# Kernel optimization log

Measured on AMD Instinct MI355X. Metric: run time of the kernel, lower is better.

The kernel has to match this reference:

```python
import jax, jax.numpy as jnp
import numpy as np

B, C, H, W = 32, 3, 256, 256
P = 32        # patch_size
NP = 4        # num_patches
STRENGTH = 0.1  # adversarial_strength default


def _conv2d(x, w, b):
    # NCHW conv, 3x3, stride 1, padding 1 ('SAME')
    y = jax.lax.conv_general_dilated(
        x, w, window_strides=(1, 1), padding='SAME',
        dimension_numbers=('NCHW', 'OIHW', 'NCHW'))
    return y + b[None, :, None, None]


def setup_inputs() -> dict:
    key = jax.random.key(0)
    ks = jax.random.split(key, 12)
    s = 0.05
    return {
        'x':   jax.random.normal(ks[0], (B, C, H, W), jnp.float32),
        # selected bit-width patch generator (bits_8): conv C->32->16->C
        'w1':  jax.random.normal(ks[1], (32, C, 3, 3), jnp.float32) * s,
        'b1':  jnp.zeros((32,), jnp.float32),
        'w2':  jax.random.normal(ks[2], (16, 32, 3, 3), jnp.float32) * s,
        'b2':  jnp.zeros((16,), jnp.float32),
        'w3':  jax.random.normal(ks[3], (C, 16, 3, 3), jnp.float32) * s,
        'b3':  jnp.zeros((C,), jnp.float32),
        # position predictor: Linear(C*64 -> 128) then Linear(128 -> NP*2)
        'pw1': jax.random.normal(ks[4], (128, C * 64), jnp.float32) * s,
        'pb1': jnp.zeros((128,), jnp.float32),
        'pw2': jax.random.normal(ks[5], (NP * 2, 128), jnp.float32) * s,
        'pb2': jnp.zeros((NP * 2,), jnp.float32),
        'bit_width': 8,
    }


def reference(x, w1, b1, w2, b2, w3, b3, pw1, pb1, pw2, pb2, bit_width):
    # patch generator for the selected bit width (bit_width selects a ModuleDict
    # entry in torch; all entries have identical structure, one set of weights here)
    h1 = jax.nn.relu(_conv2d(x, w1, b1))          # [B,32,H,W]
    h2 = jax.nn.relu(_conv2d(h1, w2, b2))         # [B,16,H,W]
    patches = jnp.tanh(_conv2d(h2, w3, b3)) * STRENGTH  # [B,C,H,W]

    # position predictor: AdaptiveAvgPool2d((8,8)) -> flatten -> MLP -> sigmoid
    pooled = x.reshape(B, C, 8, H // 8, 8, W // 8).mean(axis=(3, 5))  # [B,C,8,8]
    feat = pooled.reshape(B, -1)                                       # [B,C*64]
    hmid = jax.nn.relu(feat @ pw1.T + pb1)
    pos = jax.nn.sigmoid(hmid @ pw2.T + pb2).reshape(B, NP, 2)

    # int() truncation of sigmoid-scaled positions (nonnegative -> floor)
    y0 = jnp.floor(pos[..., 0] * (H - P)).astype(jnp.int32)  # [B,NP]
    x0 = jnp.floor(pos[..., 1] * (W - P)).astype(jnp.int32)  # [B,NP]

    ar = jnp.arange(P, dtype=jnp.int32)
    rows = y0[:, :, None, None] + ar[None, None, :, None]    # [B,NP,P,P]
    cols = x0[:, :, None, None] + ar[None, None, None, :]    # [B,NP,P,P]
    bidx = jnp.arange(B, dtype=jnp.int32)[:, None, None, None]  # [B,1,1,1]

    # gather patch values at the same windows, then scatter-add into x.
    # advanced idx (bidx, rows, cols) around the channel slice -> [B,NP,P,P,C];
    # duplicate (overlapping) windows accumulate, matching sequential += in torch.
    vals = patches[bidx, :, rows, cols]
    patched_x = x.at[bidx, :, rows, cols].add(vals)
    return patched_x
```

## Files before the change

### kernel.cpp

```cpp
#include <hip/hip_runtime.h>
#include <math.h>

#define BATCH 32
#define CH 3
#define HH 256
#define WW 256
#define PP 32
#define NPATCH 4

typedef __attribute__((ext_vector_type(8))) short short8;
typedef __attribute__((ext_vector_type(4))) float f32x4;

__device__ __forceinline__ unsigned short f2bf(float f) {
  union { float f; unsigned u; } cv;
  cv.f = f;
  unsigned u = cv.u;
  u += 0x7FFFu + ((u >> 16) & 1u);
  return (unsigned short)(u >> 16);
}

__global__ __launch_bounds__(256) void prep_kernel(
    const float* __restrict__ x, float* __restrict__ out,
    float* __restrict__ feat, const float* __restrict__ w1,
    const float* __restrict__ w2, const float* __restrict__ w3,
    const float* __restrict__ pw1, unsigned short* __restrict__ w1f,
    unsigned short* __restrict__ w2f, unsigned short* __restrict__ w3f,
    float* __restrict__ pw1t) {
  const int blk = blockIdx.x;
  const int t = threadIdx.x;

  if (blk >= 792) {
    const int seg = blk - 792;
#pragma unroll
    for (int q = 0; q < 4; ++q) {
      int idx = seg * 1024 + q * 256 + t;
      if (idx < 1024) {
        int nt = idx >> 9, lane_ = (idx >> 3) & 63, j = idx & 7;
        int lrow_ = lane_ & 15, lgrp_ = lane_ >> 4;
        int k = lgrp_ * 8 + j;
        w1f[idx] = f2bf(k < 27 ? w1[(nt * 16 + lrow_) * 27 + k] : 0.f);
      } else if (idx < 5632) {
        int id2 = idx - 1024;
        int tap = id2 >> 9, lane_ = (id2 >> 3) & 63, j = id2 & 7;
        int lrow_ = lane_ & 15, lgrp_ = lane_ >> 4;
        w2f[id2] = f2bf(w2[lrow_ * 288 + (lgrp_ * 8 + j) * 9 + tap]);
      } else if (idx < 8192) {
        int id3 = idx - 5632;
        int kk = id3 >> 9, lane_ = (id3 >> 3) & 63, j = id3 & 7;
        int lrow_ = lane_ & 15, lgrp_ = lane_ >> 4;
        int tap = 2 * kk + (lgrp_ >> 1);
        int c2 = (lgrp_ & 1) * 8 + j;
        float v = (lrow_ < 3 && tap < 9) ? w3[lrow_ * 144 + c2 * 9 + tap] : 0.f;
        w3f[id3] = f2bf(v);
      }
    }
    return;
  }

  if (blk >= 768) {
    const int tile = blk - 768;
    const int ko = (tile % 6) * 32;
    const int to = (tile / 6) * 32;
    __shared__ float tl[32][33];
    int ty = t >> 5, tx = t & 31;
#pragma unroll
    for (int r = 0; r < 4; ++r) {
      int row = r * 8 + ty;
      tl[row][tx] = pw1[(to + row) * 192 + ko + tx];
    }
    __syncthreads();
#pragma unroll
    for (int r = 0; r < 4; ++r) {
      int row = r * 8 + ty;
      pw1t[(ko + row) * 128 + to + tx] = tl[tx][row];
    }
    return;
  }

  const int b = blk / 24;
  const int rem = blk - b * 24;
  const int c = rem >> 3;
  const int i = rem & 7;
  const int wv = t >> 6;
  const int lane = t & 63;
  const int j = lane >> 3;

  __shared__ float part[32];

  const size_t base4 = ((size_t)((b * 3 + c) * 256 + i * 32)) * 64;
  float s = 0.f;
#pragma unroll
  for (int k = 0; k < 8; ++k) {
    int r = k * 4 + wv;
    size_t F = base4 + (size_t)r * 64 + lane;
    float4 v = ((const float4*)x)[F];
    ((float4*)out)[F] = v;
    s += v.x + v.y + v.z + v.w;
  }
  s += __shfl_xor(s, 1, 64);
  s += __shfl_xor(s, 2, 64);
  s += __shfl_xor(s, 4, 64);
  if ((lane & 7) == 0) part[wv * 8 + j] = s;
  __syncthreads();
  if (t < 8) {
    float tot = part[t] + part[8 + t] + part[16 + t] + part[24 + t];
    feat[b * 192 + c * 64 + i * 8 + t] = tot * (1.f / 1024.f);
  }
}

__global__ __launch_bounds__(256) void mlp_kernel(
    const float* __restrict__ feat, const float* __restrict__ pw1t,
    const float* __restrict__ pb1, const float* __restrict__ pw2,
    const float* __restrict__ pb2, int* __restrict__ posw) {
  const int b = blockIdx.x;
  const int t = threadIdx.x;
  __shared__ float fs[192];
  __shared__ float part[2][128];
  __shared__ float hs[128];

  if (t < 192) fs[t] = feat[b * 192 + t];
  __syncthreads();

  {
    const int u = t & 127, h = t >> 7;
    float a0 = 0.f, a1 = 0.f;
    const float* wp = pw1t + (h * 96) * 128 + u;
    const float* fp = fs + h * 96;
#pragma unroll 12
    for (int k = 0; k < 96; k += 2) {
      a0 = fmaf(fp[k], wp[k * 128], a0);
      a1 = fmaf(fp[k + 1], wp[(k + 1) * 128], a1);
    }
    part[h][u] = a0 + a1;
  }
  __syncthreads();
  if (t < 128) hs[t] = fmaxf(part[0][t] + part[1][t] + pb1[t], 0.f);
  __syncthreads();

  const int wv = t >> 6, hl = (t >> 5) & 1, l = t & 31;
  const int jj = wv * 2 + hl;
  float a = 0.f;
#pragma unroll
  for (int q = 0; q < 4; ++q)
    a = fmaf(hs[q * 32 + l], pw2[jj * 128 + q * 32 + l], a);
#pragma unroll
  for (int m = 1; m <= 16; m <<= 1) a += __shfl_xor(a, m, 32);
  if (l == 0) {
    float a2 = a + pb2[jj];
    float sgm = 1.f / (1.f + expf(-a2));
    posw[b * 8 + jj] = (int)floorf(sgm * (float)(HH - PP));
  }
}

__global__ __launch_bounds__(512, 4) void patch_kernel(
    const float* __restrict__ x, float* __restrict__ out,
    const float* __restrict__ b1, const float* __restrict__ b2,
    const float* __restrict__ b3, const int* __restrict__ posw,
    const unsigned short* __restrict__ w1f, const unsigned short* __restrict__ w2f,
    const unsigned short* __restrict__ w3f) {
  const int blk = blockIdx.x;
  const int s = blk & 3;
  const int p = (blk >> 2) & 3;
  const int b = blk >> 4;
  const int rb = s * 8;
  const int t = threadIdx.x;
  const int wv = t >> 6;
  const int lane = t & 63;
  const int lrow = lane & 15;
  const int lgrp = lane >> 4;

  __shared__ __align__(16) float xs[3][532];
  __shared__ __align__(16) unsigned short buf[432 * 40];
  __shared__ __align__(16) unsigned short h2ls[352 * 16];

  const int y0 = posw[b * 8 + p * 2 + 0];
  const int x0 = posw[b * 8 + p * 2 + 1];

#pragma unroll
  for (int k = 0; k < 4; ++k) {
    int idx = t + 512 * k;
    if (idx < 1596) {
      int c = idx / 532;
      int r = idx - c * 532;
      int ky = r / 38, kx = r - (r / 38) * 38;
      int gy = y0 + rb - 3 + ky, gx = x0 - 3 + kx;
      float v = 0.f;
      if ((unsigned)gy < 256u && (unsigned)gx < 256u)
        v = x[((size_t)(b * 3 + c) * 256 + gy) * 256 + gx];
      xs[c][r] = v;
    }
  }

  short8 b1f[2], b2f[9], b3f[5];
#pragma unroll
  for (int nt = 0; nt < 2; ++nt)
    b1f[nt] = *(const short8*)&w1f[(nt * 64 + lane) * 8];
#pragma unroll
  for (int tap = 0; tap < 9; ++tap)
    b2f[tap] = *(const short8*)&w2f[(tap * 64 + lane) * 8];
#pragma unroll
  for (int kk = 0; kk < 5; ++kk)
    b3f[kk] = *(const short8*)&w3f[(kk * 64 + lane) * 8];
  float b1v0 = b1[lrow], b1v1 = b1[16 + lrow];
  float bias2 = b2[lrow];
  float bias3 = (lrow < 3) ? b3[lrow] : 0.f;

  __syncthreads();

  if (t < 432) {
    int pos = t;
    int jy = pos / 36, jx = pos - (pos / 36) * 36;
    unsigned short cv[32];
#pragma unroll
    for (int c = 0; c < 3; ++c)
#pragma unroll
      for (int dy = 0; dy < 3; ++dy)
#pragma unroll
        for (int dx = 0; dx < 3; ++dx)
          cv[c * 9 + dy * 3 + dx] = f2bf(xs[c][(jy + dy) * 38 + (jx + dx)]);
#pragma unroll
    for (int k = 27; k < 32; ++k) cv[k] = 0;
#pragma unroll
    for (int qq = 0; qq < 4; ++qq) {
      short8 v8;
#pragma unroll
      for (int j = 0; j < 8; ++j) v8[j] = (short)cv[qq * 8 + j];
      *(short8*)&buf[pos * 40 + qq * 8] = v8;
    }
  }
  __syncthreads();

  f32x4 acc1[4][2];
#pragma unroll
  for (int i = 0; i < 4; ++i) {
    int mt = wv + 8 * i;
    if (mt < 27) {
      short8 a = *(const short8*)&buf[(mt * 16 + lrow) * 40 + lgrp * 8];
      f32x4 z = f32x4{0.f, 0.f, 0.f, 0.f};
#pragma unroll
      for (int nt = 0; nt < 2; ++nt)
        acc1[i][nt] = __builtin_amdgcn_mfma_f32_16x16x32_bf16(a, b1f[nt], z, 0, 0, 0);
    }
  }
  __syncthreads();

#pragma unroll
  for (int i = 0; i < 4; ++i) {
    int mt = wv + 8 * i;
    if (mt < 27) {
#pragma unroll
      for (int r = 0; r < 4; ++r) {
        int pos = mt * 16 + lgrp * 4 + r;
        int jy = pos / 36, jx = pos - (pos / 36) * 36;
        bool inim = ((unsigned)(y0 + rb - 2 + jy) < 256u) &&
                    ((unsigned)(x0 - 2 + jx) < 256u);
#pragma unroll
        for (int nt = 0; nt < 2; ++nt) {
          float v = fmaxf(acc1[i][nt][r] + (nt ? b1v1 : b1v0), 0.f);
          buf[pos * 40 + nt * 16 + lrow] = inim ? f2bf(v) : (unsigned short)0;
        }
      }
    }
  }
  __syncthreads();

  f32x4 acc[3];
#pragma unroll
  for (int i = 0; i < 3; ++i) {
    int mt = wv + 8 * i;
    if (mt < 22) {
      int pos = mt * 16 + lrow;
      int posc = pos < 340 ? pos : 339;
      int iy = posc / 34, ix = posc - (posc / 34) * 34;
      const unsigned short* abase = &buf[(iy * 36 + ix) * 40 + lgrp * 8];
      f32x4 c = f32x4{0.f, 0.f, 0.f, 0.f};
#pragma unroll
      for (int dy = 0; dy < 3; ++dy)
#pragma unroll
        for (int dx = 0; dx < 3; ++dx) {
          short8 a = *(const short8*)(abase + (dy * 36 + dx) * 40);
          c = __builtin_amdgcn_mfma_f32_16x16x32_bf16(a, b2f[dy * 3 + dx], c, 0, 0, 0);
        }
      acc[i] = c;
    } else {
      acc[i] = f32x4{0.f, 0.f, 0.f, 0.f};
    }
  }
#pragma unroll
  for (int i = 0; i < 3; ++i) {
    int mt = wv + 8 * i;
    if (mt < 22) {
#pragma unroll
      for (int r = 0; r < 4; ++r) {
        int pos = mt * 16 + lgrp * 4 + r;
        if (pos < 340) {
          int iy = pos / 34, ix = pos - (pos / 34) * 34;
          bool inim = ((unsigned)(y0 + rb - 1 + iy) < 256u) &&
                      ((unsigned)(x0 - 1 + ix) < 256u);
          float v = fmaxf(acc[i][r] + bias2, 0.f);
          h2ls[pos * 16 + lrow] = inim ? f2bf(v) : (unsigned short)0;
        }
      }
    }
  }
  __syncthreads();

  f32x4 acc3[2];
#pragma unroll
  for (int i = 0; i < 2; ++i) {
    int mt = wv * 2 + i;
    int pix = mt * 16 + lrow;
    int oy = pix >> 5, ox = pix & 31;
    f32x4 c = f32x4{0.f, 0.f, 0.f, 0.f};
#pragma unroll
    for (int kk = 0; kk < 5; ++kk) {
      int tap = 2 * kk + (lgrp >> 1);
      short8 a = short8{0, 0, 0, 0, 0, 0, 0, 0};
      if (tap < 9) {
        int dy = (tap * 11) >> 5;
        int dx = tap - dy * 3;
        a = *(const short8*)&h2ls[((oy + dy) * 34 + (ox + dx)) * 16 + (lgrp & 1) * 8];
      }
      c = __builtin_amdgcn_mfma_f32_16x16x32_bf16(a, b3f[kk], c, 0, 0, 0);
    }
    acc3[i] = c;
  }
  if (lrow < 3) {
#pragma unroll
    for (int i = 0; i < 2; ++i) {
      int mt = wv * 2 + i;
#pragma unroll
      for (int r = 0; r < 4; ++r) {
        int pix = mt * 16 + lgrp * 4 + r;
        int oy = pix >> 5, ox = pix & 31;
        float v = acc3[i][r] + bias3;
        float e = __expf(2.f * v);
        float val = (1.f - 2.f / (e + 1.f)) * 0.1f;
        atomicAdd(&out[((size_t)(b * 3 + lrow) * 256 + (y0 + rb + oy)) * 256 +
                       (x0 + ox)],
                  val);
      }
    }
  }
}

extern "C" void kernel_launch(void* const* d_in, const int* in_sizes, int n_in,
                              void* d_out, int out_size, void* d_ws, size_t ws_size,
                              hipStream_t stream) {
  const float* x   = (const float*)d_in[0];
  const float* w1  = (const float*)d_in[1];
  const float* b1  = (const float*)d_in[2];
  const float* w2  = (const float*)d_in[3];
  const float* b2  = (const float*)d_in[4];
  const float* w3  = (const float*)d_in[5];
  const float* b3  = (const float*)d_in[6];
  const float* pw1 = (const float*)d_in[7];
  const float* pb1 = (const float*)d_in[8];
  const float* pw2 = (const float*)d_in[9];
  const float* pb2 = (const float*)d_in[10];
  float* out = (float*)d_out;

  float* feat = (float*)d_ws;
  unsigned short* w1f = (unsigned short*)((char*)d_ws + 24576);
  unsigned short* w2f = (unsigned short*)((char*)d_ws + 26624);
  unsigned short* w3f = (unsigned short*)((char*)d_ws + 35840);
  float* pw1t = (float*)((char*)d_ws + 40960);
  int* posw = (int*)((char*)d_ws + 139264);

  prep_kernel<<<800, 256, 0, stream>>>(x, out, feat, w1, w2, w3, pw1,
                                       w1f, w2f, w3f, pw1t);
  mlp_kernel<<<BATCH, 256, 0, stream>>>(feat, pw1t, pb1, pw2, pb2, posw);
  patch_kernel<<<BATCH * NPATCH * 4, 512, 0, stream>>>(
      x, out, b1, b2, b3, posw, w1f, w2f, w3f);
}
```

Baseline: 31.39 us.

## Move x-to-out copy out of prep kernel into patch kernel's spare blocks

The prep kernel no longer writes the full copy of x into out; it only reads x to compute pooled features. A new small kernel initializes out only inside the patch windows (first-covering window only), and the patch kernel gets extra blocks that copy x to out everywhere outside the windows, so the bulk copy overlaps the conv work. This adds an extra kernel launch and per-element window-overlap checks, and the patch kernel's atomic or additive writes must still see initialized window regions.

```diff
diff --git a/kernel.cpp b/kernel.cpp
--- a/kernel.cpp
+++ b/kernel.cpp
@@ -20,12 +20,11 @@
 }
 
 __global__ __launch_bounds__(256) void prep_kernel(
-    const float* __restrict__ x, float* __restrict__ out,
-    float* __restrict__ feat, const float* __restrict__ w1,
-    const float* __restrict__ w2, const float* __restrict__ w3,
-    const float* __restrict__ pw1, unsigned short* __restrict__ w1f,
-    unsigned short* __restrict__ w2f, unsigned short* __restrict__ w3f,
-    float* __restrict__ pw1t) {
+    const float* __restrict__ x, float* __restrict__ feat,
+    const float* __restrict__ w1, const float* __restrict__ w2,
+    const float* __restrict__ w3, const float* __restrict__ pw1,
+    unsigned short* __restrict__ w1f, unsigned short* __restrict__ w2f,
+    unsigned short* __restrict__ w3f, float* __restrict__ pw1t) {
   const int blk = blockIdx.x;
   const int t = threadIdx.x;
 
@@ -94,7 +93,6 @@
     int r = k * 4 + wv;
     size_t F = base4 + (size_t)r * 64 + lane;
     float4 v = ((const float4*)x)[F];
-    ((float4*)out)[F] = v;
     s += v.x + v.y + v.z + v.w;
   }
   s += __shfl_xor(s, 1, 64);
@@ -152,18 +150,101 @@
   }
 }
 
-__global__ __launch_bounds__(512, 4) void patch_kernel(
+__global__ __launch_bounds__(256) void patchinit_kernel(
+    const float* __restrict__ x, float* __restrict__ out,
+    const int* __restrict__ posw) {
+  const int b = blockIdx.x;
+  const int t = threadIdx.x;
+  int wy[4], wx[4];
+#pragma unroll
+  for (int p = 0; p < 4; ++p) {
+    wy[p] = posw[b * 8 + p * 2 + 0];
+    wx[p] = posw[b * 8 + p * 2 + 1];
+  }
+#pragma unroll
+  for (int p = 0; p < 4; ++p) {
+#pragma unroll
+    for (int it = 0; it < 12; ++it) {
+      int idx = it * 256 + t;
+      int c = idx >> 10;
+      int r = idx & 1023;
+      int py = r >> 5, px = r & 31;
+      int gy = wy[p] + py, gx = wx[p] + px;
+      bool first = true;
+#pragma unroll
+      for (int pp = 0; pp < 4; ++pp)
+        if (pp < p)
+          first &= !(((unsigned)(gy - wy[pp]) < 32u) &&
+                     ((unsigned)(gx - wx[pp]) < 32u));
+      if (first) {
+        size_t o = ((size_t)(b * 3 + c) * 256 + gy) * 256 + gx;
+        out[o] = x[o];
+      }
+    }
+  }
+}
+
+__global__ __launch_bounds__(512, 4) void fused_kernel(
     const float* __restrict__ x, float* __restrict__ out,
     const float* __restrict__ b1, const float* __restrict__ b2,
     const float* __restrict__ b3, const int* __restrict__ posw,
     const unsigned short* __restrict__ w1f, const unsigned short* __restrict__ w2f,
     const unsigned short* __restrict__ w3f) {
   const int blk = blockIdx.x;
+  const int t = threadIdx.x;
+
+  if (blk >= 512) {
+    const int cb = blk - 512;
+    const int b = cb / 12;
+    const int rem = cb - b * 12;
+    const int c = rem >> 2;
+    const int q = rem & 3;
+    int wy[4], wx[4];
+#pragma unroll
+    for (int p = 0; p < 4; ++p) {
+      wy[p] = posw[b * 8 + p * 2 + 0];
+      wx[p] = posw[b * 8 + p * 2 + 1];
+    }
+    const int rl = t >> 3;
+    const int gy = q * 64 + rl;
+    const int c4b = t & 7;
+    const size_t rowoff = ((size_t)(b * 3 + c) * 256 + gy) * 256;
+    const float4* src = (const float4*)(x + rowoff);
+    float4* dst = (float4*)(out + rowoff);
+    bool rin[4];
+#pragma unroll
+    for (int p = 0; p < 4; ++p) rin[p] = (unsigned)(gy - wy[p]) < 32u;
+#pragma unroll
+    for (int k = 0; k < 8; ++k) {
+      int c4 = c4b + k * 8;
+      int gx = c4 * 4;
+      bool overlap = false;
+#pragma unroll
+      for (int p = 0; p < 4; ++p)
+        overlap |= rin[p] && (gx + 3 >= wx[p]) && (gx < wx[p] + 32);
+      float4 v = src[c4];
+      if (!overlap) {
+        dst[c4] = v;
+      } else {
+        const float* sv = (const float*)&v;
+#pragma unroll
+        for (int e = 0; e < 4; ++e) {
+          int gxe = gx + e;
+          bool inw = false;
+#pragma unroll
+          for (int p = 0; p < 4; ++p)
+            inw |= rin[p] && ((unsigned)(gxe - wx[p]) < 32u);
+          if (!inw) ((float*)dst)[c4 * 4 + e] = sv[e];
+        }
+      }
+    }
+    return;
+  }
+
   const int s = blk & 3;
   const int p = (blk >> 2) & 3;
   const int b = blk >> 4;
   const int rb = s * 8;
-  const int t = threadIdx.x;
   const int wv = t >> 6;
   const int lane = t & 63;
   const int lrow = lane & 15;
@@ -367,9 +448,10 @@
   float* pw1t = (float*)((char*)d_ws + 40960);
   int* posw = (int*)((char*)d_ws + 139264);
 
-  prep_kernel<<<800, 256, 0, stream>>>(x, out, feat, w1, w2, w3, pw1,
+  prep_kernel<<<800, 256, 0, stream>>>(x, feat, w1, w2, w3, pw1,
                                        w1f, w2f, w3f, pw1t);
   mlp_kernel<<<BATCH, 256, 0, stream>>>(feat, pw1t, pb1, pw2, pb2, posw);
-  patch_kernel<<<BATCH * NPATCH * 4, 512, 0, stream>>>(
+  patchinit_kernel<<<BATCH, 256, 0, stream>>>(x, out, posw);
+  fused_kernel<<<512 + 384, 512, 0, stream>>>(
       x, out, b1, b2, b3, posw, w1f, w2f, w3f);
 }
```

New measurement: 41.83 us. +33.3%, slower.
